# Optimization experiments

Measured on AMD Instinct MI355X. Metric: run time of the kernel, lower is better.

The kernel has to match this reference:

```python
import jax, jax.numpy as jnp
import numpy as np

B = 128                      # num_graphs (cell lines per batch)
SIZES = [706, 512, 256, 128] # nodes per graph at each level; final_node = 128
DIM = 256                    # dim_cell
DEG = 8                      # avg degree of gene-gene network
EPS = 1e-5                   # BatchNorm eps


def _build_graph():
    """Build per-graph edges (incl. self-loops, as GATConv adds) and predefined
    cluster assignments per layer, coarsening edges exactly like PyG max_pool
    (remove self-loops + coalesce). Replicated across B graphs with offsets."""
    rng = np.random.default_rng(0)
    e = rng.integers(0, SIZES[0], size=(2, SIZES[0] * DEG))
    e = e[:, e[0] != e[1]]
    e = np.unique(e, axis=1)
    edges, clusters = [], []
    cur = e
    for i in range(3):
        n_cur, n_next = SIZES[i], SIZES[i + 1]
        sl = np.arange(n_cur)
        e_sl = np.concatenate([cur, np.stack([sl, sl])], axis=1)  # add self-loops
        off = np.arange(B) * n_cur
        eg = (e_sl[:, None, :] + off[None, :, None]).reshape(2, -1)
        edges.append(eg.astype(np.int32))
        cl = np.concatenate([np.arange(n_next), rng.integers(0, n_next, size=n_cur - n_next)])
        rng.shuffle(cl)  # surjective cluster assignment n_cur -> n_next
        clg = (cl[None, :] + (np.arange(B) * n_next)[:, None]).reshape(-1)
        clusters.append(clg.astype(np.int32))
        src, dst = cl[cur[0]], cl[cur[1]]
        m = src != dst                      # pool_edge: remove self-loops
        cur = np.unique(np.stack([src[m], dst[m]]), axis=1)  # coalesce
    return edges, clusters


def setup_inputs() -> dict:
    edges, clusters = _build_graph()
    key = jax.random.key(0)
    ks = jax.random.split(key, 16)
    d = {"x": jax.random.normal(ks[0], (B * SIZES[0], 3), jnp.float32)}
    ins = [3, DIM, DIM]
    for i in range(3):
        s = 1.0 / np.sqrt(ins[i])
        a = 1.0 / np.sqrt(DIM)
        d[f"W{i}"] = jax.random.normal(ks[1 + i], (ins[i], DIM), jnp.float32) * s
        d[f"asrc{i}"] = jax.random.normal(ks[4 + i], (DIM,), jnp.float32) * a
        d[f"adst{i}"] = jax.random.normal(ks[7 + i], (DIM,), jnp.float32) * a
        d[f"b{i}"] = jnp.zeros((DIM,), jnp.float32)
        d[f"edge{i}"] = jnp.asarray(edges[i])
        d[f"cluster{i}"] = jnp.asarray(clusters[i])
    return d


def _gat(x, edge, W, a_s, a_d, b):
    """PyG GATConv, heads=1, negative_slope=0.2 (self-loops pre-added in edge)."""
    N = x.shape[0]
    h = x @ W                                    # [N, D]
    src, dst = edge[0], edge[1]
    e = jax.nn.leaky_relu((h * a_s).sum(-1)[src] + (h * a_d).sum(-1)[dst], 0.2)
    m = jax.ops.segment_max(e, dst, num_segments=N)     # segment softmax (stable)
    ex = jnp.exp(e - m[dst])
    ssum = jax.ops.segment_sum(ex, dst, num_segments=N)
    alpha = ex / ssum[dst]
    out = jax.ops.segment_sum(h[src] * alpha[:, None], dst, num_segments=N)
    return out + b


def _forward(x, Ws, a_ss, a_ds, bs, edges, clusters):
    for i in range(3):
        x = jax.nn.relu(_gat(x, edges[i], Ws[i], a_ss[i], a_ds[i], bs[i]))
        # max_pool: scatter-max over predefined clusters (coarsen nodes)
        x = jax.ops.segment_max(x, clusters[i], num_segments=B * SIZES[i + 1])
        # BatchNorm1d(affine=False), training mode: biased batch stats
        mean = x.mean(0)
        var = x.var(0)
        x = (x - mean) * jax.lax.rsqrt(var + EPS)
    return x.reshape(B, SIZES[3] * DIM)


def reference(x, W0, W1, W2, asrc0, asrc1, asrc2, adst0, adst1, adst2,
              b0, b1, b2, edge0, edge1, edge2, cluster0, cluster1, cluster2):
    return _forward(x, (W0, W1, W2), (asrc0, asrc1, asrc2), (adst0, adst1, adst2),
                    (b0, b1, b2), (edge0, edge1, edge2), (cluster0, cluster1, cluster2))
```

## Files before the change

kernel.cpp:

```cpp
#include <hip/hip_runtime.h>
#include <hip/hip_fp16.h>

#define DIM 256
#define MAXMEM 16
#define MAXDEG 288

typedef _Float16 f16x8 __attribute__((ext_vector_type(8)));
typedef float f32x4 __attribute__((ext_vector_type(4)));

__device__ inline unsigned short f2h(float f) {
  return __half_as_ushort(__float2half_rn(f));
}
__device__ inline float h2f(unsigned short u) {
  return __half2float(__ushort_as_half(u));
}
__device__ inline __half2 hmax2_(__half2 a, __half2 b) {
  __half2 c;
  c.x = __hgt(a.x, b.x) ? a.x : b.x;
  c.y = __hgt(a.y, b.y) ? a.y : b.y;
  return c;
}


struct BktArgs {
  const int* esrc[3]; const int* edst[3]; const int* cl[3];
  int Eb[3]; int est[3];
  int* bdeg[3]; int* bccnt[3]; int* bebkt[3]; int* bcbkt[3];
};

__global__ __launch_bounds__(256) void l0_fused(
    const float* __restrict__ x, const float* __restrict__ W,
    const float* __restrict__ asv, const float* __restrict__ adv,
    unsigned short* __restrict__ h, float* __restrict__ ssrc,
    float* __restrict__ sdst, int N, int Nb0, BktArgs bk, int nBkt) {
  if (blockIdx.x < (unsigned)nBkt) {
    const int NbA[3] = {706, 512, 256};
    int i = blockIdx.x * 256 + threadIdx.x;
#pragma unroll
    for (int L = 0; L < 3; L++) {
      if (i < bk.Eb[L]) {
        int d = bk.edst[L][i];
        int slot = atomicAdd(&bk.bdeg[L][d], 1);
        if (slot < bk.est[L]) bk.bebkt[L][d * bk.est[L] + slot] = bk.esrc[L][i];
      }
      if (i < NbA[L]) {
        int c = bk.cl[L][i];
        int slot = atomicAdd(&bk.bccnt[L][c], 1);
        if (slot < MAXMEM) bk.bcbkt[L][c * MAXMEM + slot] = i;
      }
    }
  }
  int wid = (blockIdx.x * 256 + threadIdx.x) >> 6;
  int lane = threadIdx.x & 63;
  if (wid >= N) return;
  int nb = wid >> 7, g = wid & 127;
  const float* xr = x + ((size_t)g * Nb0 + nb) * 3;
  float x0 = xr[0], x1 = xr[1], x2 = xr[2];
  int c = lane * 4;
  float4 w0 = *(const float4*)(W + c);
  float4 w1 = *(const float4*)(W + 256 + c);
  float4 w2 = *(const float4*)(W + 512 + c);
  float4 hv;
  hv.x = fmaf(x0, w0.x, fmaf(x1, w1.x, x2 * w2.x));
  hv.y = fmaf(x0, w0.y, fmaf(x1, w1.y, x2 * w2.y));
  hv.z = fmaf(x0, w0.z, fmaf(x1, w1.z, x2 * w2.z));
  hv.w = fmaf(x0, w0.w, fmaf(x1, w1.w, x2 * w2.w));
  ((ushort4*)(h + (size_t)wid * DIM))[lane] =
      make_ushort4(f2h(hv.x), f2h(hv.y), f2h(hv.z), f2h(hv.w));
  float4 a1 = ((const float4*)asv)[lane];
  float4 a2 = ((const float4*)adv)[lane];
  float d1 = hv.x * a1.x + hv.y * a1.y + hv.z * a1.z + hv.w * a1.w;
  float d2 = hv.x * a2.x + hv.y * a2.y + hv.z * a2.z + hv.w * a2.w;
  for (int o = 32; o > 0; o >>= 1) {
    d1 += __shfl_down(d1, o);
    d2 += __shfl_down(d2, o);
  }
  if (lane == 0) { ssrc[wid] = d1; sdst[wid] = d2; }
}

__global__ __launch_bounds__(256) void gemm_mfma(
    const unsigned short* __restrict__ A, const unsigned short* __restrict__ Wt,
    const float* __restrict__ cvec, const float* __restrict__ asv,
    const float* __restrict__ adv, unsigned short* __restrict__ H,
    float* __restrict__ ssrc, float* __restrict__ sdst, int M) {
  __shared__ unsigned short Bs[2][256 * 32];
  int tid = threadIdx.x;
  int wave = tid >> 6, lane = tid & 63;
  int m0 = blockIdx.x * 128 + wave * 32;
  int row = lane & 15, quad = lane >> 4;

#pragma unroll
  for (int i = 0; i < 4; i++) {
    int c = i * 256 + tid;
    f16x8 v = *(const f16x8*)(const void*)(Wt + (size_t)(c >> 2) * 256 + (c & 3) * 8);
    *(f16x8*)(void*)(&Bs[0][c * 8]) = v;
  }
  __syncthreads();

  const unsigned short* Ap = A + (size_t)(m0 + row) * 256 + quad * 8;
  f32x4 acc[2][16] = {};
  for (int j = 0; j < 8; j++) {
    f16x8 pf[4];
    if (j < 7) {
#pragma unroll
      for (int i = 0; i < 4; i++) {
        int c = i * 256 + tid;
        pf[i] = *(const f16x8*)(const void*)(Wt + (size_t)(c >> 2) * 256 +
                                             (j + 1) * 32 + (c & 3) * 8);
      }
    }
    f16x8 a0 = *(const f16x8*)(const void*)(Ap + j * 32);
    f16x8 a1 = *(const f16x8*)(const void*)(Ap + 16 * 256 + j * 32);
    const unsigned short* bs = Bs[j & 1];
#pragma unroll
    for (int nt = 0; nt < 16; nt++) {
      f16x8 b = *(const f16x8*)(const void*)(bs + (nt * 16 + row) * 32 + quad * 8);
      acc[0][nt] = __builtin_amdgcn_mfma_f32_16x16x32_f16(a0, b, acc[0][nt], 0, 0, 0);
      acc[1][nt] = __builtin_amdgcn_mfma_f32_16x16x32_f16(a1, b, acc[1][nt], 0, 0, 0);
    }
    if (j < 7) {
#pragma unroll
      for (int i = 0; i < 4; i++) {
        int c = i * 256 + tid;
        *(f16x8*)(void*)(&Bs[(j + 1) & 1][c * 8]) = pf[i];
      }
    }
    __syncthreads();
  }

  float sav[16], sdv[16], cv[16];
#pragma unroll
  for (int nt = 0; nt < 16; nt++) {
    sav[nt] = asv[nt * 16 + row];
    sdv[nt] = adv[nt * 16 + row];
    cv[nt] = cvec[nt * 16 + row];
  }
#pragma unroll
  for (int sub = 0; sub < 2; sub++)
#pragma unroll
    for (int r = 0; r < 4; r++) {
      int mm = m0 + sub * 16 + quad * 4 + r;
      unsigned short* out = H + (size_t)mm * 256 + row;
      float d1 = 0.f, d2 = 0.f;
#pragma unroll
      for (int nt = 0; nt < 16; nt++) {
        float hv = acc[sub][nt][r] + cv[nt];
        out[nt * 16] = f2h(hv);
        d1 = fmaf(hv, sav[nt], d1);
        d2 = fmaf(hv, sdv[nt], d2);
      }
      for (int o = 1; o < 16; o <<= 1) {
        d1 += __shfl_xor(d1, o);
        d2 += __shfl_xor(d2, o);
      }
      if (row == 0) { ssrc[mm] = d1; sdst[mm] = d2; }
    }
}

__global__ __launch_bounds__(256) void gat_fused(
    const unsigned short* __restrict__ h, const int* __restrict__ bdeg,
    const int* __restrict__ bebkt, int estride,
    const int* __restrict__ bccnt, const int* __restrict__ bcbkt,
    const float* __restrict__ ssrc, const float* __restrict__ sdst,
    const float* __restrict__ bias, unsigned short* __restrict__ pooled,
    int Mb, int lgMb) {
  __shared__ float pLDS[MAXDEG * 8];
  __shared__ float psum[8];
  int b = blockIdx.x;
  int x = b & 7, t = b >> 3;
  int c = t & (Mb - 1);
  int set = x + 8 * (t >> lgMb);
  int tid = threadIdx.x;
  int gl = tid >> 5;
  int ch = tid & 31;
  int g = set * 8 + gl;
  int nm = bccnt[c]; if (nm > MAXMEM) nm = MAXMEM;
  float4 bf0 = *(const float4*)(bias + ch * 8);
  float4 bf1 = *(const float4*)(bias + ch * 8 + 4);
  __half2 hb[4] = {__floats2half2_rn(bf0.x, bf0.y), __floats2half2_rn(bf0.z, bf0.w),
                   __floats2half2_rn(bf1.x, bf1.y), __floats2half2_rn(bf1.z, bf1.w)};
  __half2 z = __float2half2_rn(0.f);
  __half2 best[4] = {z, z, z, z};
  for (int mi = 0; mi < nm; mi++) {
    int nb = __builtin_amdgcn_readfirstlane(bcbkt[c * MAXMEM + mi]);
    int deg = __builtin_amdgcn_readfirstlane(bdeg[nb]);
    if (deg > estride) deg = estride;
    const int* bk = bebkt + nb * estride;
    if (tid < 8) psum[tid] = 0.f;
    __syncthreads();
    for (int jj = tid; jj < deg * 8; jj += 256) {
      int j = jj >> 3, gi = jj & 7;
      int g2 = set * 8 + gi;
      int s = bk[j];
      float tt = ssrc[s * 128 + g2] + sdst[nb * 128 + g2];
      tt = tt > 0.f ? tt : 0.2f * tt;
      float p = __expf(tt);
      pLDS[jj] = p;
      atomicAdd(&psum[gi], p);
    }
    __syncthreads();
    float inv = 1.f / psum[gl];
    __half2 acc[4] = {z, z, z, z};
    int j = 0;
    for (; j + 4 <= deg; j += 4) {
      int4 ss = *(const int4*)(bk + j);
      __half2 hq0 = __float2half2_rn(pLDS[(j + 0) * 8 + gl] * inv);
      __half2 hq1 = __float2half2_rn(pLDS[(j + 1) * 8 + gl] * inv);
      __half2 hq2 = __float2half2_rn(pLDS[(j + 2) * 8 + gl] * inv);
      __half2 hq3 = __float2half2_rn(pLDS[(j + 3) * 8 + gl] * inv);
      uint4 v0 = *(const uint4*)(h + ((size_t)ss.x * 128 + g) * DIM + ch * 8);
      uint4 v1 = *(const uint4*)(h + ((size_t)ss.y * 128 + g) * DIM + ch * 8);
      uint4 v2 = *(const uint4*)(h + ((size_t)ss.z * 128 + g) * DIM + ch * 8);
      uint4 v3 = *(const uint4*)(h + ((size_t)ss.w * 128 + g) * DIM + ch * 8);
      union { uint4 u; __half2 p[4]; } u0, u1, u2, u3;
      u0.u = v0; u1.u = v1; u2.u = v2; u3.u = v3;
#pragma unroll
      for (int i = 0; i < 4; i++) {
        acc[i] = __hfma2(u0.p[i], hq0, acc[i]);
        acc[i] = __hfma2(u1.p[i], hq1, acc[i]);
        acc[i] = __hfma2(u2.p[i], hq2, acc[i]);
        acc[i] = __hfma2(u3.p[i], hq3, acc[i]);
      }
    }
    for (; j < deg; j++) {
      int s = bk[j];
      __half2 hq = __float2half2_rn(pLDS[j * 8 + gl] * inv);
      uint4 v0 = *(const uint4*)(h + ((size_t)s * 128 + g) * DIM + ch * 8);
      union { uint4 u; __half2 p[4]; } u0; u0.u = v0;
#pragma unroll
      for (int i = 0; i < 4; i++) acc[i] = __hfma2(u0.p[i], hq, acc[i]);
    }
#pragma unroll
    for (int i = 0; i < 4; i++)
      best[i] = hmax2_(best[i], __hadd2(acc[i], hb[i]));
    __syncthreads();
  }
  union { uint4 u; __half2 p[4]; } o;
#pragma unroll
  for (int i = 0; i < 4; i++) o.p[i] = best[i];
  *(uint4*)(pooled + ((size_t)c * 128 + g) * DIM + ch * 8) = o.u;
}

__global__ __launch_bounds__(256) void stats_k(
    const unsigned short* __restrict__ x, float* __restrict__ sums,
    float* __restrict__ sqs, int M, const float* __restrict__ Wn,
    unsigned short* __restrict__ Wt, float* __restrict__ cvec,
    int* __restrict__ done, int do_prep) {
  int tid = threadIdx.x;
  int ch = tid & 31;
  int rg = tid >> 5;
  float s[8] = {}, q[8] = {};
  for (int r = blockIdx.x * 8 + rg; r < M; r += gridDim.x * 8) {
    uint4 v = *(const uint4*)(x + (size_t)r * DIM + ch * 8);
    union { uint4 u; __half2 p[4]; } uu; uu.u = v;
#pragma unroll
    for (int i = 0; i < 4; i++) {
      float2 f = __half22float2(uu.p[i]);
      s[2 * i]     += f.x; q[2 * i]     = fmaf(f.x, f.x, q[2 * i]);
      s[2 * i + 1] += f.y; q[2 * i + 1] = fmaf(f.y, f.y, q[2 * i + 1]);
    }
  }
  __shared__ float sm[512];
  sm[tid] = 0.f; sm[tid + 256] = 0.f;
  __syncthreads();
#pragma unroll
  for (int i = 0; i < 8; i++) {
    atomicAdd(&sm[ch * 8 + i], s[i]);
    atomicAdd(&sm[256 + ch * 8 + i], q[i]);
  }
  __syncthreads();
  atomicAdd(&sums[tid], sm[tid]);
  atomicAdd(&sqs[tid], sm[tid + 256]);

  if (!do_prep) return;
  __shared__ int lastFlag;
  __syncthreads();
  if (tid == 0) {
    __threadfence();
    lastFlag = (atomicAdd(done, 1) == (int)gridDim.x - 1);
  }
  __syncthreads();
  if (!lastFlag) return;
  __threadfence();
  float invN = 1.f / (float)M;
  {
    float mu = sums[tid] * invN;
    float var = sqs[tid] * invN - mu * mu;
    sm[tid] = mu;
    sm[256 + tid] = rsqrtf(var + 1e-5f);
  }
  __syncthreads();
  int n = tid;
  float cv = 0.f;
  for (int k = 0; k < 256; k++) {
    float w = Wn[(size_t)k * 256 + n] * sm[256 + k];
    Wt[(size_t)n * 256 + k] = f2h(w);
    cv = fmaf(sm[k], w, cv);
  }
  cvec[n] = -cv;
}

__global__ void norm_out(const unsigned short* __restrict__ xin,
                         float* __restrict__ xout,
                         const float* __restrict__ sums, const float* __restrict__ sqs,
                         float invN, int Mb, int total) {
  int idx = blockIdx.x * 256 + threadIdx.x;
  if (idx >= total) return;
  int ch = idx & 255;
  int r = idx >> 8;
  int g = r & 127, c = r >> 7;
  float mu = sums[ch] * invN;
  float var = sqs[ch] * invN - mu * mu;
  float v = (h2f(xin[idx]) - mu) * rsqrtf(var + 1e-5f);
  xout[((size_t)g * Mb + c) * 256 + ch] = v;
}

extern "C" void kernel_launch(void* const* d_in, const int* in_sizes, int n_in,
                              void* d_out, int out_size, void* d_ws, size_t ws_size,
                              hipStream_t stream) {
  const int B = 128;
  const int Nb[4] = {706, 512, 256, 128};
  const int Ns[4] = {128 * 706, 128 * 512, 128 * 256, 128 * 128};
  const int lgMb[3] = {9, 8, 7};
  const int EST[3] = {64, 160, 288};

  int iW[3], iA[3], iD[3], iB_[3], iE[3], iC[3];
  if (in_sizes[2] == 256) {
    for (int i = 0; i < 3; i++) {
      iW[i] = 1 + 6 * i; iA[i] = 2 + 6 * i; iD[i] = 3 + 6 * i;
      iB_[i] = 4 + 6 * i; iE[i] = 5 + 6 * i; iC[i] = 6 + 6 * i;
    }
  } else {
    for (int i = 0; i < 3; i++) {
      iW[i] = 1 + i; iA[i] = 4 + i; iD[i] = 7 + i;
      iB_[i] = 10 + i; iE[i] = 13 + i; iC[i] = 16 + i;
    }
  }
  int E[3];
  for (int i = 0; i < 3; i++) E[i] = in_sizes[iE[i]] / 2;

  int bebktOff[3], bcbktOff[3];
  size_t bebktTot = 0, bcbktTot = 0;
  for (int i = 0; i < 3; i++) {
    bebktOff[i] = (int)bebktTot; bebktTot += (size_t)Nb[i] * EST[i];
    bcbktOff[i] = (int)bcbktTot; bcbktTot += (size_t)Nb[i + 1] * MAXMEM;
  }

  char* wsp = (char*)d_ws;
  size_t o = 0;
  auto alloc = [&](size_t bytes) -> void* {
    void* p = wsp + o;
    o = (o + bytes + 255) & ~(size_t)255;
    return p;
  };
  unsigned short* h      = (unsigned short*)alloc((size_t)Ns[0] * DIM * 2);
  unsigned short* pooled = (unsigned short*)alloc((size_t)Ns[1] * DIM * 2);
  float* ssrc   = (float*)alloc((size_t)Ns[0] * 4);
  float* sdst   = (float*)alloc((size_t)Ns[0] * 4);
  float* statbuf= (float*)alloc(3 * 512 * 4);
  int*   bmeta  = (int*)alloc((size_t)3 * (Nb[0] + Nb[1]) * 4);
  int*   done   = (int*)alloc(16 * 4);
  char*  zend   = wsp + o;
  int*   bebkt  = (int*)alloc(bebktTot * 4);
  int*   bcbkt  = (int*)alloc(bcbktTot * 4);
  unsigned short* Wt = (unsigned short*)alloc(256 * 256 * 2);
  float* cvec   = (float*)alloc(256 * 4);
  (void)ws_size; (void)n_in; (void)out_size;

  const float* xin = (const float*)d_in[0];

  hipMemsetAsync(statbuf, 0, (size_t)(zend - (char*)statbuf), stream);

  BktArgs ba;
  int maxNeed = 0;
  for (int L = 0; L < 3; L++) {
    int Eb = E[L] / B;
    ba.esrc[L] = (const int*)d_in[iE[L]];
    ba.edst[L] = ba.esrc[L] + E[L];
    ba.cl[L]   = (const int*)d_in[iC[L]];
    ba.Eb[L] = Eb; ba.est[L] = EST[L];
    ba.bdeg[L]  = bmeta + L * (Nb[0] + Nb[1]);
    ba.bccnt[L] = ba.bdeg[L] + Nb[L];
    ba.bebkt[L] = bebkt + bebktOff[L];
    ba.bcbkt[L] = bcbkt + bcbktOff[L];
    int need = Eb > Nb[L] ? Eb : Nb[L];
    if (need > maxNeed) maxNeed = need;
  }
  int nBkt = (maxNeed + 255) / 256;

  l0_fused<<<(Ns[0] + 3) / 4, 256, 0, stream>>>(
      xin, (const float*)d_in[iW[0]], (const float*)d_in[iA[0]],
      (const float*)d_in[iD[0]], h, ssrc, sdst, Ns[0], Nb[0], ba, nBkt);

  for (int L = 0; L < 3; L++) {
    int M = Ns[L + 1];
    const float* av = (const float*)d_in[iA[L]];
    const float* dv = (const float*)d_in[iD[L]];
    const float* bv = (const float*)d_in[iB_[L]];
    int* bdeg = bmeta + L * (Nb[0] + Nb[1]);
    int* bccnt = bdeg + Nb[L];
    int* beb = bebkt + bebktOff[L];
    int* bcb = bcbkt + bcbktOff[L];
    float* sums = statbuf + L * 512;
    float* sqs  = sums + 256;

    if (L > 0) {
      gemm_mfma<<<Ns[L] / 128, 256, 0, stream>>>(pooled, Wt, cvec, av, dv,
                                                 h, ssrc, sdst, Ns[L]);
    }

    gat_fused<<<Nb[L + 1] * 16, 256, 0, stream>>>(h, bdeg, beb, EST[L],
                                                  bccnt, bcb, ssrc, sdst, bv,
                                                  pooled, Nb[L + 1], lgMb[L]);

    const float* Wn = (L < 2) ? (const float*)d_in[iW[L + 1]] : nullptr;
    stats_k<<<512, 256, 0, stream>>>(pooled, sums, sqs, M, Wn, Wt, cvec,
                                     done + L, (L < 2) ? 1 : 0);
  }

  norm_out<<<((size_t)Ns[3] * DIM + 255) / 256, 256, 0, stream>>>(
      pooled, (float*)d_out, statbuf + 2 * 512, statbuf + 2 * 512 + 256,
      1.0f / (float)Ns[3], Nb[3], Ns[3] * DIM);
}
```

Before: 370.9 us.

## Move weight-prep out of stats last-block into a parallel prep kernel

The BatchNorm-folded weight transpose and bias vector used to be computed by the single last-finishing block of stats_k, which looped serially over 256 rows. That work now runs in a separate prep_k kernel with 256 blocks, each using a shared-memory tree reduction for one output column. The done-counter and threadfence logic are removed, and the stats_k grid is doubled to 1024 blocks. The cost is two extra kernel launches per forward pass.

```diff
diff --git a/kernel.cpp b/kernel.cpp
--- a/kernel.cpp
+++ b/kernel.cpp
@@ -76,6 +76,27 @@
     d2 += __shfl_down(d2, o);
   }
   if (lane == 0) { ssrc[wid] = d1; sdst[wid] = d2; }
+}
+
+__global__ __launch_bounds__(256) void prep_k(
+    const float* __restrict__ W, const float* __restrict__ sums,
+    const float* __restrict__ sqs, float invN,
+    unsigned short* __restrict__ Wt, float* __restrict__ cvec) {
+  int n = blockIdx.x;
+  int k = threadIdx.x;
+  float mu = sums[k] * invN;
+  float var = sqs[k] * invN - mu * mu;
+  float istd = rsqrtf(var + 1e-5f);
+  float w = W[(size_t)k * 256 + n] * istd;
+  Wt[(size_t)n * 256 + k] = f2h(w);
+  __shared__ float red[256];
+  red[k] = mu * w;
+  __syncthreads();
+  for (int s = 128; s > 0; s >>= 1) {
+    if (k < s) red[k] += red[k + s];
+    __syncthreads();
+  }
+  if (k == 0) cvec[n] = -red[0];
 }
 
 __global__ __launch_bounds__(256) void gemm_mfma(
@@ -243,9 +264,7 @@
 
 __global__ __launch_bounds__(256) void stats_k(
     const unsigned short* __restrict__ x, float* __restrict__ sums,
-    float* __restrict__ sqs, int M, const float* __restrict__ Wn,
-    unsigned short* __restrict__ Wt, float* __restrict__ cvec,
-    int* __restrict__ done, int do_prep) {
+    float* __restrict__ sqs, int M) {
   int tid = threadIdx.x;
   int ch = tid & 31;
   int rg = tid >> 5;
@@ -271,33 +290,6 @@
   __syncthreads();
   atomicAdd(&sums[tid], sm[tid]);
   atomicAdd(&sqs[tid], sm[tid + 256]);
-
-  if (!do_prep) return;
-  __shared__ int lastFlag;
-  __syncthreads();
-  if (tid == 0) {
-    __threadfence();
-    lastFlag = (atomicAdd(done, 1) == (int)gridDim.x - 1);
-  }
-  __syncthreads();
-  if (!lastFlag) return;
-  __threadfence();
-  float invN = 1.f / (float)M;
-  {
-    float mu = sums[tid] * invN;
-    float var = sqs[tid] * invN - mu * mu;
-    sm[tid] = mu;
-    sm[256 + tid] = rsqrtf(var + 1e-5f);
-  }
-  __syncthreads();
-  int n = tid;
-  float cv = 0.f;
-  for (int k = 0; k < 256; k++) {
-    float w = Wn[(size_t)k * 256 + n] * sm[256 + k];
-    Wt[(size_t)n * 256 + k] = f2h(w);
-    cv = fmaf(sm[k], w, cv);
-  }
-  cvec[n] = -cv;
 }
 
 __global__ void norm_out(const unsigned short* __restrict__ xin,
@@ -359,7 +351,6 @@
   float* sdst   = (float*)alloc((size_t)Ns[0] * 4);
   float* statbuf= (float*)alloc(3 * 512 * 4);
   int*   bmeta  = (int*)alloc((size_t)3 * (Nb[0] + Nb[1]) * 4);
-  int*   done   = (int*)alloc(16 * 4);
   char*  zend   = wsp + o;
   int*   bebkt  = (int*)alloc(bebktTot * 4);
   int*   bcbkt  = (int*)alloc(bcbktTot * 4);
@@ -405,6 +396,10 @@
     float* sqs  = sums + 256;
 
     if (L > 0) {
+      float* psums = statbuf + (L - 1) * 512;
+      prep_k<<<256, 256, 0, stream>>>((const float*)d_in[iW[L]], psums,
+                                      psums + 256, 1.0f / (float)Ns[L],
+                                      Wt, cvec);
       gemm_mfma<<<Ns[L] / 128, 256, 0, stream>>>(pooled, Wt, cvec, av, dv,
                                                  h, ssrc, sdst, Ns[L]);
     }
@@ -413,9 +408,7 @@
                                                   bccnt, bcb, ssrc, sdst, bv,
                                                   pooled, Nb[L + 1], lgMb[L]);
 
-    const float* Wn = (L < 2) ? (const float*)d_in[iW[L + 1]] : nullptr;
-    stats_k<<<512, 256, 0, stream>>>(pooled, sums, sqs, M, Wn, Wt, cvec,
-                                     done + L, (L < 2) ? 1 : 0);
+    stats_k<<<1024, 256, 0, stream>>>(pooled, sums, sqs, M);
   }
 
   norm_out<<<((size_t)Ns[3] * DIM + 255) / 256, 256, 0, stream>>>(
```

Result: no change. 371.1 us (+0.1%).
